# Optimization experiments

Measured on AMD Instinct MI355X. Metric: run time of the kernel, lower is better.

Reference implementation:

```python
import jax, jax.numpy as jnp
import numpy as np

NUM_HEAD = 16
D_MODEL = 1024
D_HEAD = D_MODEL // NUM_HEAD
BATCH = 4
SEQ = 2048


def setup_inputs() -> dict:
    key = jax.random.key(0)
    kq, kk, kv, kw, kb = jax.random.split(key, 5)
    Q = jax.random.normal(kq, (BATCH, SEQ, D_MODEL), dtype=jnp.float32)
    K = jax.random.normal(kk, (BATCH, SEQ, D_MODEL), dtype=jnp.float32)
    V = jax.random.normal(kv, (BATCH, SEQ, D_MODEL), dtype=jnp.float32)
    # nn.Linear weight [out, in] and bias [out]; scaled like torch default init
    Wq_w = jax.random.normal(kw, (D_MODEL, D_MODEL), dtype=jnp.float32) * (1.0 / np.sqrt(D_MODEL))
    Wq_b = jax.random.normal(kb, (D_MODEL,), dtype=jnp.float32) * 0.01
    return {"Q": Q, "K": K, "V": V, "Wq_w": Wq_w, "Wq_b": Wq_b}


def _split_head(x):
    # [b, s, d_model] -> [b, h, s, d_head]
    b, s, _ = x.shape
    return x.reshape(b, s, NUM_HEAD, D_HEAD).transpose(0, 2, 1, 3)


def reference(Q, K, V, Wq_w, Wq_b):
    # NOTE: original module (faithfully) uses Wq for all three projections.
    q = Q @ Wq_w.T + Wq_b
    k = K @ Wq_w.T + Wq_b
    v = V @ Wq_w.T + Wq_b
    q = _split_head(q)  # [b, h, s, dh]
    k = _split_head(k)
    v = _split_head(v)
    scale = 1.0 / jnp.sqrt(jnp.float32(D_HEAD))
    scores = jnp.einsum("bhqd,bhkd->bhqk", q, k) * scale  # [b, h, s, s]
    att_w = jax.nn.softmax(scores, axis=-1)
    out = jnp.einsum("bhqk,bhkd->bhqd", att_w, v)
    out = out.transpose(0, 2, 1, 3).reshape(Q.shape[0], -1, D_MODEL)
    return out, att_w
```

## Files before the change

### kernel.cpp

```cpp
#include <hip/hip_runtime.h>

typedef _Float16 f16;
typedef _Float16 f16x8 __attribute__((ext_vector_type(8)));
typedef _Float16 f16x4 __attribute__((ext_vector_type(4)));
typedef float    f32x4 __attribute__((ext_vector_type(4)));

static constexpr int NBATCH = 4;
static constexpr int NH     = 16;
static constexpr int SQ     = 2048;
static constexpr int DM     = 1024;
static constexpr int DHEAD  = 64;
static constexpr size_t TEL = (size_t)NBATCH * SQ * DM;
static constexpr size_t WEL = (size_t)DM * DM;

static constexpr float QSCALE = 0.125f * 1.4426950408889634f;

#define MFMA32(a, b, c) __builtin_amdgcn_mfma_f32_16x16x32_f16((a), (b), (c), 0, 0, 0)
#define MFMA16(a, b, c) __builtin_amdgcn_mfma_f32_16x16x16f16((a), (b), (c), 0, 0, 0)
#define EXP2(x) __builtin_amdgcn_exp2f(x)

#define GLOAD_LDS16(g, l)                                        \
    __builtin_amdgcn_global_load_lds(                            \
        (const __attribute__((address_space(1))) void*)(g),      \
        (__attribute__((address_space(3))) void*)(l), 16, 0, 0)

__global__ __launch_bounds__(256) void cvt_kernel(
    const float* __restrict__ X0, const float* __restrict__ X1,
    const float* __restrict__ X2, const float* __restrict__ W,
    f16* __restrict__ y0, f16* __restrict__ y1,
    f16* __restrict__ y2, f16* __restrict__ yw)
{
    constexpr int CX = (int)(TEL / 8);
    constexpr int CW = (int)(WEL / 8);
    const int total = 3 * CX + CW;
    for (int c = blockIdx.x * blockDim.x + threadIdx.x; c < total;
         c += gridDim.x * blockDim.x) {
        const float* src; f16* dst; int off;
        if (c < CX)            { src = X0; dst = y0; off = c; }
        else if (c < 2 * CX)   { src = X1; dst = y1; off = c - CX; }
        else if (c < 3 * CX)   { src = X2; dst = y2; off = c - 2 * CX; }
        else                   { src = W;  dst = yw; off = c - 3 * CX; }
        const float* p = src + (size_t)off * 8;
        float4 lo = *(const float4*)p;
        float4 hi = *(const float4*)(p + 4);
        f16x8 v;
        v[0] = (f16)lo.x; v[1] = (f16)lo.y; v[2] = (f16)lo.z; v[3] = (f16)lo.w;
        v[4] = (f16)hi.x; v[5] = (f16)hi.y; v[6] = (f16)hi.z; v[7] = (f16)hi.w;
        *(f16x8*)(dst + (size_t)off * 8) = v;
    }
}

template <bool QK>
__global__ __launch_bounds__(256, 2) void proj_kernel(
    const f16* __restrict__ X0, const f16* __restrict__ X1,
    const f16* __restrict__ W, const float* __restrict__ bias,
    f16* __restrict__ d0, f16* __restrict__ d1)
{
    alignas(16) __shared__ f16 la[2][128 * 32];
    alignas(16) __shared__ f16 lb[2][128 * 32];

    const int bid   = blockIdx.x;
    const int which = QK ? (bid >> 9) : 0;
    const int t0    = bid & 511;
    const int nb    = t0 >> 6;
    const int mb    = t0 & 63;
    const f16* __restrict__ X  = (QK && which) ? X1 : X0;
    const f16* __restrict__ A0 = X + (size_t)mb * 128 * DM;
    const f16* __restrict__ B0 = W + (size_t)nb * 128 * DM;

    const int tid  = threadIdx.x;
    const int wave = tid >> 6;
    const int lane = tid & 63;
    const int wr   = wave >> 1, wc = wave & 1;
    const int l16  = lane & 15, g = lane >> 4;
    const int m_base = mb * 128 + wr * 64;
    const int n_base = nb * 128 + wc * 64;

    auto stage = [&](int buf, int k0) {
        #pragma unroll
        for (int half = 0; half < 2; ++half) {
            const int idx = half * 256 + wave * 64 + lane;
            const int row = idx >> 2;
            const int sc  = (idx & 3) ^ ((row >> 1) & 3);
            const int db  = (half * 256 + wave * 64) * 8;
            GLOAD_LDS16(A0 + (size_t)row * DM + k0 + sc * 8, &la[buf][db]);
            GLOAD_LDS16(B0 + (size_t)row * DM + k0 + sc * 8, &lb[buf][db]);
        }
    };

    f32x4 acc[4][4];
    #pragma unroll
    for (int i = 0; i < 4; ++i)
        #pragma unroll
        for (int j = 0; j < 4; ++j)
            acc[i][j] = (f32x4){0.f, 0.f, 0.f, 0.f};

    stage(0, 0);
    __syncthreads();
    for (int t = 0; t < 32; ++t) {
        const int buf = t & 1;
        if (t < 31) stage(buf ^ 1, (t + 1) * 32);
        f16x8 af[4], bf[4];
        #pragma unroll
        for (int qs = 0; qs < 4; ++qs) {
            const int row = wr * 64 + qs * 16 + l16;
            af[qs] = *(const f16x8*)&la[buf][row * 32 +
                                             ((g ^ ((row >> 1) & 3)) << 3)];
        }
        #pragma unroll
        for (int ns = 0; ns < 4; ++ns) {
            const int row = wc * 64 + ns * 16 + l16;
            bf[ns] = *(const f16x8*)&lb[buf][row * 32 +
                                             ((g ^ ((row >> 1) & 3)) << 3)];
        }
        #pragma unroll
        for (int qs = 0; qs < 4; ++qs)
            #pragma unroll
            for (int ns = 0; ns < 4; ++ns)
                acc[qs][ns] = QK ? MFMA32(bf[ns], af[qs], acc[qs][ns])
                                 : MFMA32(af[qs], bf[ns], acc[qs][ns]);
        __syncthreads();
    }

    const int    s_base = m_base & (SQ - 1);
    const int    b      = m_base >> 11;
    const int    h      = nb * 2 + wc;
    const size_t bh     = (size_t)b * NH + h;

    if (QK) {
        f16* __restrict__ dst = which ? d1 : d0;
        const float sc = (which == 0) ? QSCALE : 1.0f;
        #pragma unroll
        for (int qs = 0; qs < 4; ++qs) {
            const int s = s_base + qs * 16 + l16;
            #pragma unroll
            for (int ns = 0; ns < 4; ++ns) {
                float4 bb = *(const float4*)&bias[n_base + ns * 16 + 4 * g];
                f16x4 pk;
                pk[0] = (f16)((acc[qs][ns][0] + bb.x) * sc);
                pk[1] = (f16)((acc[qs][ns][1] + bb.y) * sc);
                pk[2] = (f16)((acc[qs][ns][2] + bb.z) * sc);
                pk[3] = (f16)((acc[qs][ns][3] + bb.w) * sc);
                *(f16x4*)(dst + (bh * SQ + s) * DHEAD + ns * 16 + 4 * g) = pk;
            }
        }
    } else {
        float bv[4];
        #pragma unroll
        for (int ns = 0; ns < 4; ++ns) bv[ns] = bias[n_base + ns * 16 + l16];
        #pragma unroll
        for (int qs = 0; qs < 4; ++qs)
            #pragma unroll
            for (int ns = 0; ns < 4; ++ns) {
                f16x4 pk;
                #pragma unroll
                for (int r = 0; r < 4; ++r) pk[r] = (f16)(acc[qs][ns][r] + bv[ns]);
                const int dh = ns * 16 + l16;
                const int s0 = s_base + qs * 16 + 4 * g;
                *(f16x4*)(d0 + (bh * DHEAD + dh) * SQ + s0) = pk;
            }
    }
}

__global__ __launch_bounds__(256, 4) void attn_kernel(
    const f16* __restrict__ wq, const f16* __restrict__ wk,
    const f16* __restrict__ wv,
    float* __restrict__ out, float* __restrict__ att)
{
    alignas(16) __shared__ f16 lk[2][64 * 64];
    alignas(16) __shared__ f16 lv[2][64 * 64];

    const int tid  = threadIdx.x;
    const int wave = tid >> 6;
    const int lane = tid & 63;
    const int l16  = lane & 15, g = lane >> 4;

    const int bid     = blockIdx.x;
    const int logical = (bid & 7) * 128 + (bid >> 3);
    const int bh      = logical >> 4;
    const int q0      = (logical & 15) * 128 + wave * 32;

    const f16* __restrict__ qp = wq + (size_t)bh * SQ * DHEAD;
    const f16* __restrict__ kp = wk + (size_t)bh * SQ * DHEAD;
    const f16* __restrict__ vp = wv + (size_t)bh * DHEAD * SQ;
    float* __restrict__ attp = att + ((size_t)bh * SQ + q0) * SQ;
    const int b = bh >> 4, h = bh & 15;
    float* __restrict__ outp = out + ((size_t)b * SQ + q0) * DM + h * DHEAD;

    auto stage64 = [&](f16* dst0, const f16* gbase, int stride) {
        #pragma unroll
        for (int half = 0; half < 2; ++half) {
            const int idx = half * 256 + wave * 64 + lane;
            const int row = idx >> 3;
            const int sc  = (idx & 7) ^ (row & 7);
            GLOAD_LDS16(gbase + (size_t)row * stride + sc * 8,
                        dst0 + (size_t)(half * 256 + wave * 64) * 8);
        }
    };
    auto ldk8 = [&](int buf, int row, int c) -> f16x8 {
        return *(const f16x8*)&lk[buf][row * 64 + ((c ^ (row & 7)) << 3)];
    };
    auto ldv4 = [&](int buf, int row, int c_lin, int half8) -> f16x4 {
        return *(const f16x4*)&lv[buf][row * 64 + ((c_lin ^ (row & 7)) << 3) +
                                       half8 * 4];
    };

    f16x8 qf[2][2];
    #pragma unroll
    for (int qs = 0; qs < 2; ++qs)
        #pragma unroll
        for (int dhf = 0; dhf < 2; ++dhf)
            qf[qs][dhf] = *(const f16x8*)(qp + (size_t)(q0 + qs * 16 + l16) * DHEAD +
                                          dhf * 32 + g * 8);

    const f32x4 zero = (f32x4){0.f, 0.f, 0.f, 0.f};
    constexpr int NT = SQ / 64;

    float accl[2] = {0.f, 0.f};
    f32x4 oacc[2][4];
    #pragma unroll
    for (int qs = 0; qs < 2; ++qs)
        #pragma unroll
        for (int ds = 0; ds < 4; ++ds) oacc[qs][ds] = zero;

    stage64(&lk[0][0], kp, DHEAD);
    stage64(&lv[0][0], vp, SQ);
    __syncthreads();
    for (int t = 0; t < NT; ++t) {
        const int buf = t & 1;
        if (t + 1 < NT) {
            stage64(&lk[buf ^ 1][0], kp + (size_t)(t + 1) * 64 * DHEAD, DHEAD);
            stage64(&lv[buf ^ 1][0], vp + (t + 1) * 64, SQ);
        }
        #pragma unroll
        for (int s16 = 0; s16 < 4; ++s16) {
            const int row = s16 * 16 + l16;
            f16x8 kf0 = ldk8(buf, row, g);
            f16x8 kf1 = ldk8(buf, row, 4 + g);
            f16x4 pb[2];
            #pragma unroll
            for (int qs = 0; qs < 2; ++qs) {
                f32x4 sc = MFMA32(kf0, qf[qs][0], zero);
                sc = MFMA32(kf1, qf[qs][1], sc);
                float e0 = EXP2(sc[0]), e1 = EXP2(sc[1]);
                float e2 = EXP2(sc[2]), e3 = EXP2(sc[3]);
                accl[qs] += (e0 + e1) + (e2 + e3);
                f16x4 p; p[0] = (f16)e0; p[1] = (f16)e1;
                p[2] = (f16)e2; p[3] = (f16)e3;
                pb[qs] = p;
            }
            #pragma unroll
            for (int ds = 0; ds < 4; ++ds) {
                f16x4 vf = ldv4(buf, ds * 16 + l16, s16 * 2 + (g >> 1), g & 1);
                oacc[0][ds] = MFMA16(vf, pb[0], oacc[0][ds]);
                oacc[1][ds] = MFMA16(vf, pb[1], oacc[1][ds]);
            }
        }
        __syncthreads();
    }

    float linv[2];
    #pragma unroll
    for (int qs = 0; qs < 2; ++qs) {
        float v = accl[qs];
        v += __shfl_xor(v, 16, 64);
        v += __shfl_xor(v, 32, 64);
        linv[qs] = 1.f / v;
    }

    #pragma unroll
    for (int qs = 0; qs < 2; ++qs)
        #pragma unroll
        for (int ds = 0; ds < 4; ++ds) {
            float4 o;
            o.x = oacc[qs][ds][0] * linv[qs];
            o.y = oacc[qs][ds][1] * linv[qs];
            o.z = oacc[qs][ds][2] * linv[qs];
            o.w = oacc[qs][ds][3] * linv[qs];
            *(float4*)(outp + (size_t)(qs * 16 + l16) * DM + ds * 16 + 4 * g) = o;
        }

    stage64(&lk[0][0], kp, DHEAD);
    __syncthreads();
    for (int t = 0; t < NT; ++t) {
        const int buf = t & 1;
        const int kv0 = t * 64;
        if (t + 1 < NT)
            stage64(&lk[buf ^ 1][0], kp + (size_t)(t + 1) * 64 * DHEAD, DHEAD);
        #pragma unroll
        for (int s16 = 0; s16 < 4; ++s16) {
            const int row = s16 * 16 + l16;
            f16x8 kf0 = ldk8(buf, row, g);
            f16x8 kf1 = ldk8(buf, row, 4 + g);
            #pragma unroll
            for (int qs = 0; qs < 2; ++qs) {
                f32x4 sc = MFMA32(kf0, qf[qs][0], zero);
                sc = MFMA32(kf1, qf[qs][1], sc);
                float4 a;
                a.x = EXP2(sc[0]) * linv[qs];
                a.y = EXP2(sc[1]) * linv[qs];
                a.z = EXP2(sc[2]) * linv[qs];
                a.w = EXP2(sc[3]) * linv[qs];
                *(float4*)(attp + (size_t)(qs * 16 + l16) * SQ + kv0 +
                           s16 * 16 + 4 * g) = a;
            }
        }
        __syncthreads();
    }
}

extern "C" void kernel_launch(void* const* d_in, const int* in_sizes, int n_in,
                              void* d_out, int out_size, void* d_ws, size_t ws_size,
                              hipStream_t stream) {
    const float* Q    = (const float*)d_in[0];
    const float* K    = (const float*)d_in[1];
    const float* V    = (const float*)d_in[2];
    const float* W    = (const float*)d_in[3];
    const float* bias = (const float*)d_in[4];

    f16* wq = (f16*)d_ws;
    f16* wk = wq + TEL;
    f16* wv = wk + TEL;

    float* out = (float*)d_out;
    float* att = out + TEL;

    f16* x0 = (f16*)att;
    f16* x1 = x0 + TEL;
    f16* x2 = x1 + TEL;
    f16* xw = x2 + TEL;

    cvt_kernel <<<2048, 256, 0, stream>>>(Q, K, V, W, x0, x1, x2, xw);
    proj_kernel<true ><<<1024, 256, 0, stream>>>(x0, x1, xw, bias, wq, wk);
    proj_kernel<false><<< 512, 256, 0, stream>>>(x2, nullptr, xw, bias, wv, nullptr);
    attn_kernel<<<1024, 256, 0, stream>>>(wq, wk, wv, out, att);
}
```

Before: 443.8 us.

## Use 16x16x32 MFMA for PV product and single barrier per tile

The PV product now pairs two 16-key slices so each MFMA uses the K=32 f16 instruction instead of two K=16 ones, halving the PV MFMA count. The k-dimension ordering stays consistent because the P fragments and V fragments are packed the same way. The loop also moves to one barrier per tile, an explicit vmcnt wait before the s_barrier, which replaces the trailing __syncthreads and the pre-loop sync. This cuts synchronization points but relies on global_load_lds completion being tracked by vmcnt.

```diff
diff --git a/kernel.cpp b/kernel.cpp
--- a/kernel.cpp
+++ b/kernel.cpp
@@ -16,7 +16,6 @@
 static constexpr float QSCALE = 0.125f * 1.4426950408889634f;
 
 #define MFMA32(a, b, c) __builtin_amdgcn_mfma_f32_16x16x32_f16((a), (b), (c), 0, 0, 0)
-#define MFMA16(a, b, c) __builtin_amdgcn_mfma_f32_16x16x16f16((a), (b), (c), 0, 0, 0)
 #define EXP2(x) __builtin_amdgcn_exp2f(x)
 
 #define GLOAD_LDS16(g, l)                                        \
@@ -225,38 +224,47 @@
 
     stage64(&lk[0][0], kp, DHEAD);
     stage64(&lv[0][0], vp, SQ);
-    __syncthreads();
     for (int t = 0; t < NT; ++t) {
         const int buf = t & 1;
+        asm volatile("s_waitcnt vmcnt(0)" ::: "memory");
+        __builtin_amdgcn_s_barrier();
         if (t + 1 < NT) {
             stage64(&lk[buf ^ 1][0], kp + (size_t)(t + 1) * 64 * DHEAD, DHEAD);
             stage64(&lv[buf ^ 1][0], vp + (t + 1) * 64, SQ);
         }
         #pragma unroll
-        for (int s16 = 0; s16 < 4; ++s16) {
-            const int row = s16 * 16 + l16;
-            f16x8 kf0 = ldk8(buf, row, g);
-            f16x8 kf1 = ldk8(buf, row, 4 + g);
-            f16x4 pb[2];
-            #pragma unroll
-            for (int qs = 0; qs < 2; ++qs) {
-                f32x4 sc = MFMA32(kf0, qf[qs][0], zero);
-                sc = MFMA32(kf1, qf[qs][1], sc);
-                float e0 = EXP2(sc[0]), e1 = EXP2(sc[1]);
-                float e2 = EXP2(sc[2]), e3 = EXP2(sc[3]);
-                accl[qs] += (e0 + e1) + (e2 + e3);
-                f16x4 p; p[0] = (f16)e0; p[1] = (f16)e1;
-                p[2] = (f16)e2; p[3] = (f16)e3;
-                pb[qs] = p;
+        for (int p = 0; p < 2; ++p) {
+            f16x8 pb8[2];
+            #pragma unroll
+            for (int hh = 0; hh < 2; ++hh) {
+                const int row = p * 32 + hh * 16 + l16;
+                f16x8 kf0 = ldk8(buf, row, g);
+                f16x8 kf1 = ldk8(buf, row, 4 + g);
+                #pragma unroll
+                for (int qs = 0; qs < 2; ++qs) {
+                    f32x4 sc = MFMA32(kf0, qf[qs][0], zero);
+                    sc = MFMA32(kf1, qf[qs][1], sc);
+                    float e0 = EXP2(sc[0]), e1 = EXP2(sc[1]);
+                    float e2 = EXP2(sc[2]), e3 = EXP2(sc[3]);
+                    accl[qs] += (e0 + e1) + (e2 + e3);
+                    pb8[qs][hh * 4 + 0] = (f16)e0;
+                    pb8[qs][hh * 4 + 1] = (f16)e1;
+                    pb8[qs][hh * 4 + 2] = (f16)e2;
+                    pb8[qs][hh * 4 + 3] = (f16)e3;
+                }
             }
             #pragma unroll
             for (int ds = 0; ds < 4; ++ds) {
-                f16x4 vf = ldv4(buf, ds * 16 + l16, s16 * 2 + (g >> 1), g & 1);
-                oacc[0][ds] = MFMA16(vf, pb[0], oacc[0][ds]);
-                oacc[1][ds] = MFMA16(vf, pb[1], oacc[1][ds]);
-            }
-        }
-        __syncthreads();
+                const int vrow = ds * 16 + l16;
+                f16x4 va = ldv4(buf, vrow, p * 4 + (g >> 1), g & 1);
+                f16x4 vb = ldv4(buf, vrow, p * 4 + 2 + (g >> 1), g & 1);
+                f16x8 vf8;
+                vf8[0] = va[0]; vf8[1] = va[1]; vf8[2] = va[2]; vf8[3] = va[3];
+                vf8[4] = vb[0]; vf8[5] = vb[1]; vf8[6] = vb[2]; vf8[7] = vb[3];
+                oacc[0][ds] = MFMA32(vf8, pb8[0], oacc[0][ds]);
+                oacc[1][ds] = MFMA32(vf8, pb8[1], oacc[1][ds]);
+            }
+        }
     }
 
     float linv[2];
```

After: 435.6 us. Within noise of the previous version (-1.8%).
